# Optimization experiments

Hardware: AMD Instinct MI355X
Metric: run time of the kernel (lower is better)

The kernel has to match this reference:

```python
import jax, jax.numpy as jnp
from jax import lax
import numpy as np

_CUBIC = np.array([-0.01171875, -0.03515625, 0.11328125, 0.43359375,
                   0.43359375, 0.11328125, -0.03515625, -0.01171875], dtype=np.float32)


def setup_inputs() -> dict:
    key = jax.random.key(0)
    x = jax.random.normal(key, (4, 64, 128, 4096), dtype=jnp.float32)
    kernel = jnp.asarray(_CUBIC)  # fixed anti-aliasing FIR buffer (K=8)
    return {"x": x, "kernel": kernel}


def reference(x, kernel):
    # Downsample-by-2 along T with depthwise cubic FIR (diagonal weight in the
    # original => exactly a per-channel 1D convolution).
    B, C0, Fbins, T = x.shape
    K = kernel.shape[0]
    pad = K // 2 - 1  # 3 for cubic
    xr = x.reshape(-1, Fbins, T)                                  # (B*C0, F, T)
    xp = jnp.pad(xr, ((0, 0), (0, 0), (pad, pad)), mode="reflect")
    w = jnp.broadcast_to(kernel, (Fbins, 1, K))                   # depthwise OIW
    y = lax.conv_general_dilated(
        xp, w,
        window_strides=(2,),
        padding="VALID",
        dimension_numbers=("NCH", "OIH", "NCH"),
        feature_group_count=Fbins,
    )                                                             # (B*C0, F, T/2)
    return y.reshape(B, -1, Fbins, y.shape[-1])
```

## Files before the change

### kernel.cpp

```cpp
#include <hip/hip_runtime.h>


#define TLEN 4096
#define OLEN 2048
#define NTHREADS 256
#define NROWS 32768

typedef float f4 __attribute__((ext_vector_type(4)));
typedef float f2 __attribute__((ext_vector_type(2)));

__global__ __launch_bounds__(NTHREADS) void fir_down2_poly(
    const float* __restrict__ x, const float* __restrict__ w,
    float* __restrict__ y)
{
    __shared__ __align__(16) float Ebuf[2052];
    __shared__ __align__(16) float Obuf[2052];

    const int tid = threadIdx.x;
    const long row = blockIdx.x;
    const f4* __restrict__ x4 = (const f4*)(x + row * (long)TLEN);
    f4* __restrict__ y4 = (f4*)(y + row * (long)OLEN);

    const float k0=w[0],k1=w[1],k2=w[2],k3=w[3],k4=w[4],k5=w[5],k6=w[6],k7=w[7];

#pragma unroll
    for (int j = 0; j < 4; ++j) {
        const int i = tid + j * NTHREADS;
        const f4 v = __builtin_nontemporal_load(&x4[i]);
        *(f2*)&Ebuf[2*i+2] = (f2){v.y, v.w};
        *(f2*)&Obuf[2*i+2] = (f2){v.x, v.z};
        if (i == 0) {
            Ebuf[0] = v.w;
            Ebuf[1] = v.y;
            Obuf[1] = v.z;
            Obuf[0] = 0.f;
        }
        if (i == 1023) {
            Ebuf[2050] = v.y;
            Obuf[2050] = v.z;
            Obuf[2051] = v.x;
            Ebuf[2051] = 0.f;
        }
    }
    __syncthreads();

    const f4* E4 = (const f4*)Ebuf;
    const f4* O4 = (const f4*)Obuf;
#pragma unroll
    for (int g = 0; g < 2; ++g) {
        const int u = tid + g * NTHREADS;
        const f4 eA = E4[u], eB = E4[u + 1];
        const f4 oA = O4[u], oB = O4[u + 1];
        const float Ev[7] = {eA.x, eA.y, eA.z, eA.w, eB.x, eB.y, eB.z};
        const float Ov[7] = {oA.y, oA.z, oA.w, oB.x, oB.y, oB.z, oB.w};
        float o[4];
#pragma unroll
        for (int r = 0; r < 4; ++r)
            o[r] = Ev[r] * k0 + Ov[r] * k1 + Ev[r+1] * k2 + Ov[r+1] * k3
                 + Ev[r+2] * k4 + Ov[r+2] * k5 + Ev[r+3] * k6 + Ov[r+3] * k7;
        const f4 out = {o[0], o[1], o[2], o[3]};
        __builtin_nontemporal_store(out, &y4[u]);
    }
}

extern "C" void kernel_launch(void* const* d_in, const int* in_sizes, int n_in,
                              void* d_out, int out_size, void* d_ws, size_t ws_size,
                              hipStream_t stream) {
    const float* x = (const float*)d_in[0];
    const float* w = (const float*)d_in[1];
    float* y = (float*)d_out;
    fir_down2_poly<<<NROWS, NTHREADS, 0, stream>>>(x, w, y);
}
```

Before: 131.9 us.

## Give each wavefront a private LDS slice with halo loads to drop block barrier

The row is now split into four independent wavefront-owned segments. Each wavefront de-interleaves its segment into its own LDS slice and fetches its neighbour boundary samples straight from global memory. This replaces the block-wide __syncthreads with a per-wave LDS waitcnt, so waves no longer stall on each other. In exchange it adds a few extra edge global loads and relies on in-wave LDS ordering for correctness.

```diff
diff --git a/kernel.cpp b/kernel.cpp
--- a/kernel.cpp
+++ b/kernel.cpp
@@ -9,46 +9,48 @@
 typedef float f4 __attribute__((ext_vector_type(4)));
 typedef float f2 __attribute__((ext_vector_type(2)));
 
-__global__ __launch_bounds__(NTHREADS) void fir_down2_poly(
+__global__ __launch_bounds__(NTHREADS) void fir_down2_wavepriv(
     const float* __restrict__ x, const float* __restrict__ w,
     float* __restrict__ y)
 {
-    __shared__ __align__(16) float Ebuf[2052];
-    __shared__ __align__(16) float Obuf[2052];
+    __shared__ __align__(16) float Eb[4][520];
+    __shared__ __align__(16) float Ob[4][520];
 
     const int tid = threadIdx.x;
+    const int wv = tid >> 6;
+    const int lane = tid & 63;
     const long row = blockIdx.x;
     const f4* __restrict__ x4 = (const f4*)(x + row * (long)TLEN);
-    f4* __restrict__ y4 = (f4*)(y + row * (long)OLEN);
+    f4* __restrict__ y4 = (f4*)(y + row * (long)OLEN) + 128 * wv;
 
     const float k0=w[0],k1=w[1],k2=w[2],k3=w[3],k4=w[4],k5=w[5],k6=w[6],k7=w[7];
 
+    float* __restrict__ Ew = Eb[wv];
+    float* __restrict__ Ow = Ob[wv];
+
+    f4 v[4];
 #pragma unroll
     for (int j = 0; j < 4; ++j) {
-        const int i = tid + j * NTHREADS;
-        const f4 v = __builtin_nontemporal_load(&x4[i]);
-        *(f2*)&Ebuf[2*i+2] = (f2){v.y, v.w};
-        *(f2*)&Obuf[2*i+2] = (f2){v.x, v.z};
-        if (i == 0) {
-            Ebuf[0] = v.w;
-            Ebuf[1] = v.y;
-            Obuf[1] = v.z;
-            Obuf[0] = 0.f;
-        }
-        if (i == 1023) {
-            Ebuf[2050] = v.y;
-            Obuf[2050] = v.z;
-            Obuf[2051] = v.x;
-            Ebuf[2051] = 0.f;
-        }
+        const int q = 64 * j + lane;
+        v[j] = __builtin_nontemporal_load(&x4[256 * wv + q]);
+        *(f2*)&Ew[2*q + 2] = (f2){v[j].y, v[j].w};
+        *(f2*)&Ow[2*q + 2] = (f2){v[j].x, v[j].z};
     }
-    __syncthreads();
+    if (lane == 0) {
+        if (wv == 0) { Ew[0] = v[0].w; Ew[1] = v[0].y; Ow[1] = v[0].z; }
+        else { const f4 L = x4[256*wv - 1]; Ew[0] = L.y; Ew[1] = L.w; Ow[1] = L.z; }
+    }
+    if (lane == 63) {
+        if (wv == 3) { Ew[514] = v[3].y; Ow[514] = v[3].z; Ow[515] = v[3].x; }
+        else { const f4 R = x4[256*wv + 256]; Ew[514] = R.y; Ow[514] = R.x; Ow[515] = R.z; }
+    }
+    asm volatile("s_waitcnt lgkmcnt(0)" ::: "memory");
 
-    const f4* E4 = (const f4*)Ebuf;
-    const f4* O4 = (const f4*)Obuf;
+    const f4* E4 = (const f4*)Ew;
+    const f4* O4 = (const f4*)Ow;
 #pragma unroll
     for (int g = 0; g < 2; ++g) {
-        const int u = tid + g * NTHREADS;
+        const int u = lane + 64 * g;
         const f4 eA = E4[u], eB = E4[u + 1];
         const f4 oA = O4[u], oB = O4[u + 1];
         const float Ev[7] = {eA.x, eA.y, eA.z, eA.w, eB.x, eB.y, eB.z};
@@ -69,5 +71,5 @@
     const float* x = (const float*)d_in[0];
     const float* w = (const float*)d_in[1];
     float* y = (float*)d_out;
-    fir_down2_poly<<<NROWS, NTHREADS, 0, stream>>>(x, w, y);
+    fir_down2_wavepriv<<<NROWS, NTHREADS, 0, stream>>>(x, w, y);
 }
```

New measurement: 128.6 us. 1.03x faster.
